# Performance work log

Hardware: AMD Instinct MI355X
Metric: run time of the kernel (lower is better)

Reference implementation:

```python
import jax, jax.numpy as jnp
import numpy as np

DIM = 1024
INTER = 2048
N_EXPERTS = 8
TOP_K = 2
ROUTE_SCALE = 1.0


def setup_inputs() -> dict:
    key = jax.random.key(0)
    ks = jax.random.split(key, 4)
    x = jax.random.normal(ks[0], (4, 2048, DIM), dtype=jnp.float32)
    # Gate weight matches nn.Parameter(torch.randn(n_experts, dim))
    Wg = jax.random.normal(ks[1], (N_EXPERTS, DIM), dtype=jnp.float32)
    W1 = jax.random.normal(ks[2], (N_EXPERTS, DIM, INTER), dtype=jnp.float32) * (1.0 / np.sqrt(DIM))
    b1 = jnp.zeros((N_EXPERTS, INTER), dtype=jnp.float32)
    W2 = jax.random.normal(ks[3], (N_EXPERTS, INTER, DIM), dtype=jnp.float32) * (1.0 / np.sqrt(INTER))
    b2 = jnp.zeros((N_EXPERTS, DIM), dtype=jnp.float32)
    return {"x": x, "Wg": Wg, "W1": W1, "b1": b1, "W2": W2, "b2": b2}


def reference(x, Wg, W1, b1, W2, b2):
    # Flatten tokens: [T, D]
    xt = x.reshape(-1, DIM)
    T = xt.shape[0]

    # --- Gate: sigmoid scores, top-k, normalized weights ---
    scores = jax.nn.sigmoid(xt @ Wg.T)                       # [T, E]
    top_w, top_idx = jax.lax.top_k(scores, TOP_K)            # [T, K]
    top_w = top_w / jnp.sum(top_w, axis=-1, keepdims=True)
    top_w = top_w * ROUTE_SCALE

    # Sparse combine weights [T, E] (top_k indices are distinct per token)
    cw = jnp.zeros((T, N_EXPERTS), dtype=xt.dtype)
    cw = cw.at[jnp.arange(T)[:, None], top_idx].set(top_w)

    # --- Experts: dense per-expert MLP, weighted combine ---
    # (dropout is identity in eval mode)
    h = jax.nn.relu(jnp.einsum('td,edh->eth', xt, W1) + b1[:, None, :])   # [E, T, H]
    eo = jnp.einsum('eth,ehd->etd', h, W2) + b2[:, None, :]               # [E, T, D]
    y = jnp.einsum('etd,te->td', eo, cw)                                  # [T, D]
    return y
```

## Files before the change

kernel.cpp:

```cpp
#include <hip/hip_runtime.h>
#include <stdint.h>

#define DIM   1024
#define INTER 2048
#define NEXP  8
#define TIMAX 136

typedef _Float16 f16;
typedef __attribute__((ext_vector_type(2))) _Float16 f16x2;
typedef __attribute__((ext_vector_type(4))) _Float16 f16x4;
typedef __attribute__((ext_vector_type(8))) _Float16 f16x8;
typedef __attribute__((ext_vector_type(4))) float    f32x4;

static __device__ __forceinline__ void gload16(const void* gsrc, void* lds) {
    __builtin_amdgcn_global_load_lds(
        (const __attribute__((address_space(1))) uint32_t*)gsrc,
        (__attribute__((address_space(3))) uint32_t*)lds,
        16, 0, 0);
}

__global__ void gate_convert_kernel(const float* __restrict__ x, const float* __restrict__ Wg,
                                    f16* __restrict__ xh, float* __restrict__ gw,
                                    int* __restrict__ gidx, int T) {
    const int tok  = (int)((blockIdx.x * (size_t)blockDim.x + threadIdx.x) >> 6);
    const int lane = threadIdx.x & 63;
    if (tok >= T) return;
    const float4* xr  = (const float4*)(x + (size_t)tok * DIM);
    f16*          xhr = xh + (size_t)tok * DIM;
    float s[NEXP];
    #pragma unroll
    for (int e = 0; e < NEXP; ++e) s[e] = 0.f;
    #pragma unroll
    for (int it = 0; it < 4; ++it) {
        int i = it * 64 + lane;
        float4 xv = xr[i];
        f16x4 hv = { (f16)xv.x, (f16)xv.y, (f16)xv.z, (f16)xv.w };
        *(f16x4*)(xhr + i * 4) = hv;
        #pragma unroll
        for (int e = 0; e < NEXP; ++e) {
            float4 wv = ((const float4*)(Wg + e * DIM))[i];
            s[e] += xv.x * wv.x + xv.y * wv.y + xv.z * wv.z + xv.w * wv.w;
        }
    }
    #pragma unroll
    for (int e = 0; e < NEXP; ++e) {
        #pragma unroll
        for (int off = 32; off > 0; off >>= 1) s[e] += __shfl_xor(s[e], off);
    }
    if (lane == 0) {
        float sc[NEXP];
        #pragma unroll
        for (int e = 0; e < NEXP; ++e) sc[e] = 1.f / (1.f + expf(-s[e]));
        int i0 = 0;
        #pragma unroll
        for (int e = 1; e < NEXP; ++e) if (sc[e] > sc[i0]) i0 = e;
        int i1 = -1;
        #pragma unroll
        for (int e = 0; e < NEXP; ++e) if (e != i0 && (i1 < 0 || sc[e] > sc[i1])) i1 = e;
        float w0 = sc[i0], w1 = sc[i1];
        float inv = 1.f / (w0 + w1);
        gw[2 * tok + 0] = w0 * inv;
        gw[2 * tok + 1] = w1 * inv;
        gidx[2 * tok + 0] = i0;
        gidx[2 * tok + 1] = i1;
    }
}

__global__ void transpose_conv_kernel(const float* __restrict__ W, f16* __restrict__ Wt, int K, int N) {
    __shared__ f16 tile[64][66];
    const int e  = blockIdx.z;
    const int kb = blockIdx.y * 64;
    const int nb = blockIdx.x * 64;
    const int t  = threadIdx.x;
    const float* We  = W  + (size_t)e * K * N;
    f16*         Wte = Wt + (size_t)e * K * N;
    const int kl = t >> 4;
    const int nq = t & 15;
    #pragma unroll
    for (int pass = 0; pass < 4; ++pass) {
        int k = pass * 16 + kl;
        float4 v = *(const float4*)&We[(size_t)(kb + k) * N + nb + nq * 4];
        f16x2 lo = { (f16)v.x, (f16)v.y };
        f16x2 hi = { (f16)v.z, (f16)v.w };
        *(f16x2*)&tile[k][nq * 4]     = lo;
        *(f16x2*)&tile[k][nq * 4 + 2] = hi;
    }
    __syncthreads();
    const int n  = t >> 2;
    const int kq = t & 3;
    f16x8 o0, o1;
    #pragma unroll
    for (int i = 0; i < 8; ++i) o0[i] = tile[kq * 16 + i][n];
    #pragma unroll
    for (int i = 0; i < 8; ++i) o1[i] = tile[kq * 16 + 8 + i][n];
    f16* dst = &Wte[(size_t)(nb + n) * K + kb + kq * 16];
    *(f16x8*)dst       = o0;
    *(f16x8*)(dst + 8) = o1;
}

__global__ __launch_bounds__(1024)
void route_kernel(const int* __restrict__ gidx, int* __restrict__ offsets,
                  int* __restrict__ tor, int* __restrict__ ros,
                  int* __restrict__ tileE, int* __restrict__ tileR0, int T) {
    const int tid  = threadIdx.x;
    const int lane = tid & 63;
    const int wv   = tid >> 6;
    const int NE   = 2 * T;
    __shared__ int wc[16][NEXP];
    __shared__ int rb[NEXP];

    int c[NEXP];
    #pragma unroll
    for (int e = 0; e < NEXP; ++e) c[e] = 0;
    for (int i = tid; i < NE; i += 1024) {
        int g = gidx[i];
        #pragma unroll
        for (int e = 0; e < NEXP; ++e) c[e] += (g == e) ? 1 : 0;
    }
    #pragma unroll
    for (int e = 0; e < NEXP; ++e) {
        #pragma unroll
        for (int off = 32; off > 0; off >>= 1) c[e] += __shfl_xor(c[e], off);
    }
    if (lane == 0) {
        #pragma unroll
        for (int e = 0; e < NEXP; ++e) wc[wv][e] = c[e];
    }
    __syncthreads();
    if (tid == 0) {
        int acc = 0;
        for (int e = 0; e < NEXP; ++e) {
            int t = 0;
            for (int w2 = 0; w2 < 16; ++w2) t += wc[w2][e];
            offsets[e] = acc;
            rb[e] = acc;
            acc += t;
        }
        offsets[NEXP] = acc;
        int nt = 0;
        for (int e = 0; e < NEXP; ++e)
            for (int r0 = offsets[e]; r0 < offsets[e + 1]; r0 += 128) {
                tileE[nt]  = e;
                tileR0[nt] = r0;
                ++nt;
            }
        for (; nt < TIMAX; ++nt) { tileE[nt] = -1; tileR0[nt] = 0; }
    }
    __syncthreads();

    for (int base = 0; base < NE; base += 1024) {
        int i = base + tid;
        int g = gidx[i];
        int myrank = 0;
        #pragma unroll
        for (int e = 0; e < NEXP; ++e) {
            unsigned long long m = __ballot(g == e);
            if (g == e) myrank = __popcll(m & ((1ull << lane) - 1ull));
            if (lane == 0) wc[wv][e] = __popcll(m);
        }
        __syncthreads();
        int pre = 0;
        for (int w2 = 0; w2 < wv; ++w2) pre += wc[w2][g];
        int pos = rb[g] + pre + myrank;
        tor[pos] = i >> 1;
        ros[i]   = pos;
        __syncthreads();
        if (tid < NEXP) {
            int t = 0;
            for (int w2 = 0; w2 < 16; ++w2) t += wc[w2][tid];
            rb[tid] += t;
        }
        __syncthreads();
    }
}

template<int KD, int ND, bool RELU, bool GATHER>
__global__ __launch_bounds__(256)
void moe_gemm_kernel(const f16* __restrict__ Abase, const f16* __restrict__ Bt,
                     const float* __restrict__ bias, const int* __restrict__ offsets,
                     const int* __restrict__ tok, const int* __restrict__ tileE,
                     const int* __restrict__ tileR0, f16* __restrict__ Cout) {
    constexpr int NT  = ND / 128;
    constexpr int NT2 = NT / 2;
    const int bid = blockIdx.x;
    const int xcd = bid & 7;
    const int j   = bid >> 3;
    const int nt  = (j % NT2) * 2 + (xcd & 1);
    const int tih = j / NT2;
    const int ti  = tih * 4 + (xcd >> 1);

    const int e = tileE[ti];
    if (e < 0) return;
    const int row0   = tileR0[ti];
    const int rowEnd = offsets[e + 1];
    const int n0   = nt * 128;
    const int tid  = threadIdx.x;
    const int lane = tid & 63;
    const int wid  = tid >> 6;
    const int wr   = (wid >> 1) * 64;
    const int wc   = (wid & 1) * 64;

    __shared__ __align__(16) f16 As[128 * 64];
    __shared__ __align__(16) f16 Bs[128 * 64];

    const f16* Bte = Bt + (size_t)e * ND * KD;

    int aOff[4], bOff[4], ldsOff[4];
    #pragma unroll
    for (int i = 0; i < 4; ++i) {
        int c  = i * 256 + tid;
        int r  = c >> 3;
        int kc = (c & 7) ^ (r & 7);
        ldsOff[i] = c * 8;
        int gr = row0 + r;
        if (gr >= rowEnd) gr = rowEnd - 1;
        int ar = GATHER ? tok[gr] : gr;
        aOff[i] = ar * KD + kc * 8;
        bOff[i] = (n0 + r) * KD + kc * 8;
    }

    f32x4 acc[4][4] = {};

    const int rb    = lane & 15;
    const int jbase = lane >> 4;

    constexpr int nK = KD / 64;
    for (int kt = 0; kt < nK; ++kt) {
        const int k0 = kt * 64;
        #pragma unroll
        for (int i = 0; i < 4; ++i)
            gload16(Abase + (size_t)(aOff[i] + k0), &As[ldsOff[i]]);
        #pragma unroll
        for (int i = 0; i < 4; ++i)
            gload16(Bte + (size_t)(bOff[i] + k0), &Bs[ldsOff[i]]);
        __syncthreads();

        #pragma unroll
        for (int ks = 0; ks < 2; ++ks) {
            const int sl = (((ks * 4 + jbase) ^ (rb & 7))) * 8;
            f16x8 af[4], bfr[4];
            #pragma unroll
            for (int m = 0; m < 4; ++m)
                af[m] = *(const f16x8*)&As[(wr + m * 16 + rb) * 64 + sl];
            #pragma unroll
            for (int n = 0; n < 4; ++n)
                bfr[n] = *(const f16x8*)&Bs[(wc + n * 16 + rb) * 64 + sl];
            #pragma unroll
            for (int m = 0; m < 4; ++m)
                #pragma unroll
                for (int n = 0; n < 4; ++n)
                    acc[m][n] = __builtin_amdgcn_mfma_f32_16x16x32_f16(af[m], bfr[n], acc[m][n], 0, 0, 0);
        }

        __syncthreads();
    }

    const int rowsValid = rowEnd - row0;
    #pragma unroll
    for (int m = 0; m < 4; ++m) {
        #pragma unroll
        for (int n = 0; n < 4; ++n) {
            #pragma unroll
            for (int j2 = 0; j2 < 4; ++j2) {
                int rl  = wr + m * 16 + ((lane >> 4) << 2) + j2;
                int col = n0 + wc + n * 16 + (lane & 15);
                if (rl < rowsValid) {
                    float v = acc[m][n][j2] + bias[e * ND + col];
                    if (RELU) v = fmaxf(v, 0.f);
                    Cout[(size_t)(row0 + rl) * ND + col] = (f16)v;
                }
            }
        }
    }
}

__global__ void combine_kernel(const f16* __restrict__ eo, const int* __restrict__ ros,
                               const float* __restrict__ gw, float* __restrict__ y, int T) {
    int gid = blockIdx.x * 256 + threadIdx.x;
    int t   = gid >> 7;
    if (t >= T) return;
    int c0 = (gid & 127) * 8;
    int r0 = ros[2 * t], r1 = ros[2 * t + 1];
    float w0 = gw[2 * t], w1 = gw[2 * t + 1];
    f16x8 v0 = *(const f16x8*)(eo + (size_t)r0 * DIM + c0);
    f16x8 v1 = *(const f16x8*)(eo + (size_t)r1 * DIM + c0);
    f32x4 o0, o1;
    #pragma unroll
    for (int j = 0; j < 4; ++j) o0[j] = w0 * (float)v0[j] + w1 * (float)v1[j];
    #pragma unroll
    for (int j = 0; j < 4; ++j) o1[j] = w0 * (float)v0[4 + j] + w1 * (float)v1[4 + j];
    *(f32x4*)(y + (size_t)t * DIM + c0)     = o0;
    *(f32x4*)(y + (size_t)t * DIM + c0 + 4) = o1;
}

extern "C" void kernel_launch(void* const* d_in, const int* in_sizes, int n_in,
                              void* d_out, int out_size, void* d_ws, size_t ws_size,
                              hipStream_t stream) {
    const float* x  = (const float*)d_in[0];
    const float* Wg = (const float*)d_in[1];
    const float* W1 = (const float*)d_in[2];
    const float* b1 = (const float*)d_in[3];
    const float* W2 = (const float*)d_in[4];
    const float* b2 = (const float*)d_in[5];
    float* y = (float*)d_out;
    const int T = in_sizes[0] / DIM;

    char* ws = (char*)d_ws;
    size_t off = 0;
    auto alloc = [&](size_t bytes) -> char* {
        char* p = ws + off;
        off += (bytes + 255) & ~(size_t)255;
        return p;
    };
    f16* xh   = (f16*)alloc((size_t)T * DIM * 2);
    f16* w1t  = (f16*)alloc((size_t)NEXP * DIM * INTER * 2);
    f16* w2t  = (f16*)alloc((size_t)NEXP * DIM * INTER * 2);
    f16* h    = (f16*)alloc((size_t)2 * T * INTER * 2);
    f16* eo   = (f16*)alloc((size_t)2 * T * DIM * 2);
    float* gw = (float*)alloc((size_t)T * 2 * 4);
    int* gidx = (int*)alloc((size_t)T * 2 * 4);
    int* ros  = (int*)alloc((size_t)T * 2 * 4);
    int* tor  = (int*)alloc((size_t)2 * T * 4);
    int* offsets = (int*)alloc(64 * 4);
    int* tileE   = (int*)alloc(TIMAX * 4);
    int* tileR0  = (int*)alloc(TIMAX * 4);

    gate_convert_kernel<<<T / 4, 256, 0, stream>>>(x, Wg, xh, gw, gidx, T);
    transpose_conv_kernel<<<dim3(INTER / 64, DIM / 64, NEXP), 256, 0, stream>>>(W1, w1t, DIM, INTER);
    transpose_conv_kernel<<<dim3(DIM / 64, INTER / 64, NEXP), 256, 0, stream>>>(W2, w2t, INTER, DIM);
    route_kernel<<<1, 1024, 0, stream>>>(gidx, offsets, tor, ros, tileE, tileR0, T);
    moe_gemm_kernel<DIM, INTER, true, true>
        <<<dim3((TIMAX / 4) * ((INTER / 128) / 2) * 8), 256, 0, stream>>>(xh, w1t, b1, offsets, tor, tileE, tileR0, h);
    moe_gemm_kernel<INTER, DIM, false, false>
        <<<dim3((TIMAX / 4) * ((DIM / 128) / 2) * 8), 256, 0, stream>>>(h, w2t, b2, offsets, tor, tileE, tileR0, eo);
    combine_kernel<<<(T * DIM / 8 + 255) / 256, 256, 0, stream>>>(eo, ros, gw, y, T);
}
```

Before: 331.8 us.

## Merge preprocessing kernels and fuse weighted combine into second GEMM via atomics

Folds the gate/convert kernel and both weight transpose kernels into one launch that picks its role from the block index. The combine kernel is removed: the second expert GEMM scatters gate-weighted results straight into a zeroed fp32 output with atomicAdd, using per-row gate weights permuted during routing. This cuts launches and drops the fp16 expert-output round trip, in exchange for a memset and scalar atomics that contend when two experts update the same token.

```diff
diff --git a/kernel.cpp b/kernel.cpp
--- a/kernel.cpp
+++ b/kernel.cpp
@@ -19,59 +19,9 @@
         16, 0, 0);
 }
 
-__global__ void gate_convert_kernel(const float* __restrict__ x, const float* __restrict__ Wg,
-                                    f16* __restrict__ xh, float* __restrict__ gw,
-                                    int* __restrict__ gidx, int T) {
-    const int tok  = (int)((blockIdx.x * (size_t)blockDim.x + threadIdx.x) >> 6);
-    const int lane = threadIdx.x & 63;
-    if (tok >= T) return;
-    const float4* xr  = (const float4*)(x + (size_t)tok * DIM);
-    f16*          xhr = xh + (size_t)tok * DIM;
-    float s[NEXP];
-    #pragma unroll
-    for (int e = 0; e < NEXP; ++e) s[e] = 0.f;
-    #pragma unroll
-    for (int it = 0; it < 4; ++it) {
-        int i = it * 64 + lane;
-        float4 xv = xr[i];
-        f16x4 hv = { (f16)xv.x, (f16)xv.y, (f16)xv.z, (f16)xv.w };
-        *(f16x4*)(xhr + i * 4) = hv;
-        #pragma unroll
-        for (int e = 0; e < NEXP; ++e) {
-            float4 wv = ((const float4*)(Wg + e * DIM))[i];
-            s[e] += xv.x * wv.x + xv.y * wv.y + xv.z * wv.z + xv.w * wv.w;
-        }
-    }
-    #pragma unroll
-    for (int e = 0; e < NEXP; ++e) {
-        #pragma unroll
-        for (int off = 32; off > 0; off >>= 1) s[e] += __shfl_xor(s[e], off);
-    }
-    if (lane == 0) {
-        float sc[NEXP];
-        #pragma unroll
-        for (int e = 0; e < NEXP; ++e) sc[e] = 1.f / (1.f + expf(-s[e]));
-        int i0 = 0;
-        #pragma unroll
-        for (int e = 1; e < NEXP; ++e) if (sc[e] > sc[i0]) i0 = e;
-        int i1 = -1;
-        #pragma unroll
-        for (int e = 0; e < NEXP; ++e) if (e != i0 && (i1 < 0 || sc[e] > sc[i1])) i1 = e;
-        float w0 = sc[i0], w1 = sc[i1];
-        float inv = 1.f / (w0 + w1);
-        gw[2 * tok + 0] = w0 * inv;
-        gw[2 * tok + 1] = w1 * inv;
-        gidx[2 * tok + 0] = i0;
-        gidx[2 * tok + 1] = i1;
-    }
-}
-
-__global__ void transpose_conv_kernel(const float* __restrict__ W, f16* __restrict__ Wt, int K, int N) {
-    __shared__ f16 tile[64][66];
-    const int e  = blockIdx.z;
-    const int kb = blockIdx.y * 64;
-    const int nb = blockIdx.x * 64;
-    const int t  = threadIdx.x;
+__device__ __forceinline__ void transpose_tile(const float* __restrict__ W, f16* __restrict__ Wt,
+                                               int K, int N, int e, int kb, int nb, int t,
+                                               f16 (*tile)[66]) {
     const float* We  = W  + (size_t)e * K * N;
     f16*         Wte = Wt + (size_t)e * K * N;
     const int kl = t >> 4;
@@ -98,9 +48,76 @@
     *(f16x8*)(dst + 8) = o1;
 }
 
+__global__ void preprocess_kernel(const float* __restrict__ x, const float* __restrict__ Wg,
+                                  const float* __restrict__ W1, const float* __restrict__ W2,
+                                  f16* __restrict__ xh, f16* __restrict__ w1t, f16* __restrict__ w2t,
+                                  float* __restrict__ gw, int* __restrict__ gidx, int T) {
+    __shared__ f16 tile[64][66];
+    const int bid     = blockIdx.x;
+    const int NB_GATE = T / 4;
+    const int NB_TR1  = (INTER / 64) * (DIM / 64) * NEXP;
+
+    if (bid < NB_GATE) {
+        const int tid  = threadIdx.x;
+        const int tok  = bid * 4 + (tid >> 6);
+        const int lane = tid & 63;
+        const float4* xr  = (const float4*)(x + (size_t)tok * DIM);
+        f16*          xhr = xh + (size_t)tok * DIM;
+        float s[NEXP];
+        #pragma unroll
+        for (int e = 0; e < NEXP; ++e) s[e] = 0.f;
+        #pragma unroll
+        for (int it = 0; it < 4; ++it) {
+            int i = it * 64 + lane;
+            float4 xv = xr[i];
+            f16x4 hv = { (f16)xv.x, (f16)xv.y, (f16)xv.z, (f16)xv.w };
+            *(f16x4*)(xhr + i * 4) = hv;
+            #pragma unroll
+            for (int e = 0; e < NEXP; ++e) {
+                float4 wv = ((const float4*)(Wg + e * DIM))[i];
+                s[e] += xv.x * wv.x + xv.y * wv.y + xv.z * wv.z + xv.w * wv.w;
+            }
+        }
+        #pragma unroll
+        for (int e = 0; e < NEXP; ++e) {
+            #pragma unroll
+            for (int off = 32; off > 0; off >>= 1) s[e] += __shfl_xor(s[e], off);
+        }
+        if (lane == 0) {
+            float sc[NEXP];
+            #pragma unroll
+            for (int e = 0; e < NEXP; ++e) sc[e] = 1.f / (1.f + expf(-s[e]));
+            int i0 = 0;
+            #pragma unroll
+            for (int e = 1; e < NEXP; ++e) if (sc[e] > sc[i0]) i0 = e;
+            int i1 = -1;
+            #pragma unroll
+            for (int e = 0; e < NEXP; ++e) if (e != i0 && (i1 < 0 || sc[e] > sc[i1])) i1 = e;
+            float w0 = sc[i0], w1 = sc[i1];
+            float inv = 1.f / (w0 + w1);
+            gw[2 * tok + 0] = w0 * inv;
+            gw[2 * tok + 1] = w1 * inv;
+            gidx[2 * tok + 0] = i0;
+            gidx[2 * tok + 1] = i1;
+        }
+    } else if (bid < NB_GATE + NB_TR1) {
+        const int b  = bid - NB_GATE;
+        const int nx = b % (INTER / 64);
+        const int ky = (b / (INTER / 64)) % (DIM / 64);
+        const int e  = b / ((INTER / 64) * (DIM / 64));
+        transpose_tile(W1, w1t, DIM, INTER, e, ky * 64, nx * 64, threadIdx.x, tile);
+    } else {
+        const int b  = bid - NB_GATE - NB_TR1;
+        const int nx = b % (DIM / 64);
+        const int ky = (b / (DIM / 64)) % (INTER / 64);
+        const int e  = b / ((DIM / 64) * (INTER / 64));
+        transpose_tile(W2, w2t, INTER, DIM, e, ky * 64, nx * 64, threadIdx.x, tile);
+    }
+}
+
 __global__ __launch_bounds__(1024)
-void route_kernel(const int* __restrict__ gidx, int* __restrict__ offsets,
-                  int* __restrict__ tor, int* __restrict__ ros,
+void route_kernel(const int* __restrict__ gidx, const float* __restrict__ gw,
+                  int* __restrict__ offsets, int* __restrict__ tor, float* __restrict__ gwp,
                   int* __restrict__ tileE, int* __restrict__ tileR0, int T) {
     const int tid  = threadIdx.x;
     const int lane = tid & 63;
@@ -163,7 +180,7 @@
         for (int w2 = 0; w2 < wv; ++w2) pre += wc[w2][g];
         int pos = rb[g] + pre + myrank;
         tor[pos] = i >> 1;
-        ros[i]   = pos;
+        gwp[pos] = gw[i];
         __syncthreads();
         if (tid < NEXP) {
             int t = 0;
@@ -174,12 +191,13 @@
     }
 }
 
-template<int KD, int ND, bool RELU, bool GATHER>
+template<int KD, int ND, bool RELU, bool GATHER, bool ATOMIC>
 __global__ __launch_bounds__(256)
 void moe_gemm_kernel(const f16* __restrict__ Abase, const f16* __restrict__ Bt,
                      const float* __restrict__ bias, const int* __restrict__ offsets,
                      const int* __restrict__ tok, const int* __restrict__ tileE,
-                     const int* __restrict__ tileR0, f16* __restrict__ Cout) {
+                     const int* __restrict__ tileR0, const float* __restrict__ gwp,
+                     float* __restrict__ yout, f16* __restrict__ Cout) {
     constexpr int NT  = ND / 128;
     constexpr int NT2 = NT / 2;
     const int bid = blockIdx.x;
@@ -265,32 +283,18 @@
                 int rl  = wr + m * 16 + ((lane >> 4) << 2) + j2;
                 int col = n0 + wc + n * 16 + (lane & 15);
                 if (rl < rowsValid) {
+                    int grow = row0 + rl;
                     float v = acc[m][n][j2] + bias[e * ND + col];
                     if (RELU) v = fmaxf(v, 0.f);
-                    Cout[(size_t)(row0 + rl) * ND + col] = (f16)v;
+                    if (ATOMIC) {
+                        atomicAdd(&yout[(size_t)tok[grow] * ND + col], v * gwp[grow]);
+                    } else {
+                        Cout[(size_t)grow * ND + col] = (f16)v;
+                    }
                 }
             }
         }
     }
-}
-
-__global__ void combine_kernel(const f16* __restrict__ eo, const int* __restrict__ ros,
-                               const float* __restrict__ gw, float* __restrict__ y, int T) {
-    int gid = blockIdx.x * 256 + threadIdx.x;
-    int t   = gid >> 7;
-    if (t >= T) return;
-    int c0 = (gid & 127) * 8;
-    int r0 = ros[2 * t], r1 = ros[2 * t + 1];
-    float w0 = gw[2 * t], w1 = gw[2 * t + 1];
-    f16x8 v0 = *(const f16x8*)(eo + (size_t)r0 * DIM + c0);
-    f16x8 v1 = *(const f16x8*)(eo + (size_t)r1 * DIM + c0);
-    f32x4 o0, o1;
-    #pragma unroll
-    for (int j = 0; j < 4; ++j) o0[j] = w0 * (float)v0[j] + w1 * (float)v1[j];
-    #pragma unroll
-    for (int j = 0; j < 4; ++j) o1[j] = w0 * (float)v0[4 + j] + w1 * (float)v1[4 + j];
-    *(f32x4*)(y + (size_t)t * DIM + c0)     = o0;
-    *(f32x4*)(y + (size_t)t * DIM + c0 + 4) = o1;
 }
 
 extern "C" void kernel_launch(void* const* d_in, const int* in_sizes, int n_in,
@@ -316,22 +320,26 @@
     f16* w1t  = (f16*)alloc((size_t)NEXP * DIM * INTER * 2);
     f16* w2t  = (f16*)alloc((size_t)NEXP * DIM * INTER * 2);
     f16* h    = (f16*)alloc((size_t)2 * T * INTER * 2);
-    f16* eo   = (f16*)alloc((size_t)2 * T * DIM * 2);
     float* gw = (float*)alloc((size_t)T * 2 * 4);
+    float* gwp= (float*)alloc((size_t)T * 2 * 4);
     int* gidx = (int*)alloc((size_t)T * 2 * 4);
-    int* ros  = (int*)alloc((size_t)T * 2 * 4);
     int* tor  = (int*)alloc((size_t)2 * T * 4);
     int* offsets = (int*)alloc(64 * 4);
     int* tileE   = (int*)alloc(TIMAX * 4);
     int* tileR0  = (int*)alloc(TIMAX * 4);
 
-    gate_convert_kernel<<<T / 4, 256, 0, stream>>>(x, Wg, xh, gw, gidx, T);
-    transpose_conv_kernel<<<dim3(INTER / 64, DIM / 64, NEXP), 256, 0, stream>>>(W1, w1t, DIM, INTER);
-    transpose_conv_kernel<<<dim3(DIM / 64, INTER / 64, NEXP), 256, 0, stream>>>(W2, w2t, INTER, DIM);
-    route_kernel<<<1, 1024, 0, stream>>>(gidx, offsets, tor, ros, tileE, tileR0, T);
-    moe_gemm_kernel<DIM, INTER, true, true>
-        <<<dim3((TIMAX / 4) * ((INTER / 128) / 2) * 8), 256, 0, stream>>>(xh, w1t, b1, offsets, tor, tileE, tileR0, h);
-    moe_gemm_kernel<INTER, DIM, false, false>
-        <<<dim3((TIMAX / 4) * ((DIM / 128) / 2) * 8), 256, 0, stream>>>(h, w2t, b2, offsets, tor, tileE, tileR0, eo);
-    combine_kernel<<<(T * DIM / 8 + 255) / 256, 256, 0, stream>>>(eo, ros, gw, y, T);
-}
+    hipMemsetAsync(y, 0, (size_t)T * DIM * 4, stream);
+
+    const int NB_GATE = T / 4;
+    const int NB_TR1  = (INTER / 64) * (DIM / 64) * NEXP;
+    const int NB_TR2  = (DIM / 64) * (INTER / 64) * NEXP;
+    preprocess_kernel<<<NB_GATE + NB_TR1 + NB_TR2, 256, 0, stream>>>(
+        x, Wg, W1, W2, xh, w1t, w2t, gw, gidx, T);
+    route_kernel<<<1, 1024, 0, stream>>>(gidx, gw, offsets, tor, gwp, tileE, tileR0, T);
+    moe_gemm_kernel<DIM, INTER, true, true, false>
+        <<<dim3((TIMAX / 4) * ((INTER / 128) / 2) * 8), 256, 0, stream>>>(
+            xh, w1t, b1, offsets, tor, tileE, tileR0, nullptr, nullptr, h);
+    moe_gemm_kernel<INTER, DIM, false, false, true>
+        <<<dim3((TIMAX / 4) * ((DIM / 128) / 2) * 8), 256, 0, stream>>>(
+            h, w2t, b2, offsets, tor, tileE, tileR0, gwp, y, nullptr);
+}
```

After: 375.4 us. +13.1%, slower.
